# Optimization experiments

Hardware: AMD Instinct MI355X
Metric: run time of the kernel (lower is better)

The kernel has to match this reference:

```python
import jax, jax.numpy as jnp
import numpy as np
from itertools import permutations

SIZES = (16, 32, 32, 32)  # token_sizes for layout dims (v, t, h, w)
N = SIZES[0] * SIZES[1] * SIZES[2] * SIZES[3]  # num_tokens = 524288
B = 32
EPS = 1e-3


def setup_inputs() -> dict:
    key = jax.random.key(0)
    ks = jax.random.split(key, 12)
    u = lambda k, shape: jax.random.uniform(k, shape, dtype=jnp.float32)
    alphas = [1.0, 2.0, 4.0]
    comps = np.array(
        [[alphas[v], alphas[t], alphas[hw], alphas[hw]]
         for v, t, hw in permutations(range(3), 3)], dtype=np.float32)  # [6, 4]
    return {
        "components": jnp.asarray(comps),
        "u_rate_src": u(ks[0], (1,)),
        "u_rate_tgt": u(ks[1], (1,)),
        "u0_src": u(ks[2], (B, N)),
        "u0_tgt": u(ks[3], (B, N)),
        "u_v_src": u(ks[4], (B, SIZES[0])),
        "u_t_src": u(ks[5], (B, SIZES[1])),
        "u_h_src": u(ks[6], (B, SIZES[2])),
        "u_w_src": u(ks[7], (B, SIZES[3])),
        "u_v_tgt": u(ks[8], (B, SIZES[0])),
        "u_t_tgt": u(ks[9], (B, SIZES[1])),
        "u_h_tgt": u(ks[10], (B, SIZES[2])),
        "u_w_tgt": u(ks[11], (B, SIZES[3])),
        "idx": 2,
    }


def _clamp(x):
    return jnp.clip(x, EPS, 1.0 - EPS)


def _binary_mask(u_rate, u0, u_dims, alphas):
    # event_prior: log-prob per token = log U0 + sum_dim log(U_dim)/alpha_dim (broadcast over pattern)
    P = jnp.log(_clamp(u0))  # [B, N]
    for i, ud in enumerate(u_dims):
        shape = [B, 1, 1, 1, 1]
        shape[1 + i] = SIZES[i]
        rep = jnp.broadcast_to(
            (jnp.log(_clamp(ud)) / alphas[i]).reshape(shape),
            (B,) + SIZES).reshape(B, N)
        P = P + rep
    # rate_prior: one shared uniform, K = floor(U * N), expanded over batch
    K = (_clamp(u_rate) * N).astype(jnp.int32)  # [1]
    K = jnp.broadcast_to(K, (B,))[:, None]  # [B, 1]
    # binary_topk_: rank via double argsort (0 = largest), mask = K > rank
    rank = jnp.argsort(jnp.argsort(-P, axis=-1), axis=-1)
    return K > rank


def reference(components, u_rate_src, u_rate_tgt, u0_src, u0_tgt,
              u_v_src, u_t_src, u_h_src, u_w_src,
              u_v_tgt, u_t_tgt, u_h_tgt, u_w_tgt, idx):
    alphas = components[idx]  # [4], one alpha per layout dim, shared by src/tgt
    src = _binary_mask(u_rate_src, u0_src,
                       (u_v_src, u_t_src, u_h_src, u_w_src), alphas)
    tgt = _binary_mask(u_rate_tgt, u0_tgt,
                       (u_v_tgt, u_t_tgt, u_h_tgt, u_w_tgt), alphas)
    return src, tgt
```

## Files before the change

kernel.cpp:

```cpp
#include <hip/hip_runtime.h>
#include <stdint.h>

#define NTOK 524288
#define ROWS 64
#define CHUNKS 64
#define CHUNKS_H 32
#define NTHR 256
#define F4_PER_ROW (NTOK / 4)
#define F4_PER_CHUNK (F4_PER_ROW / CHUNKS)
#define F4_PER_THR (F4_PER_CHUNK / NTHR)
#define F4_PER_CHUNK_H (F4_PER_ROW / CHUNKS_H)
#define F4_PER_THR_H (F4_PER_CHUNK_H / NTHR)
#define NB1 2048
#define B1BASE 30720
#define BCAP 65536
#define GCAP 8192
#define STAGECAP 512

#define OFF_H16  0u
#define OFF_B1   (OFF_H16 + ROWS * NB1 * 4u)
#define OFF_CG   (OFF_B1 + 256u)
#define OFF_BCNT (OFF_CG + 256u)
#define OFF_IT   (OFF_BCNT + 256u)
#define OFF_T    (OFF_IT + 256u)
#define OFF_ZERO_END (OFF_T + 512u)
#define OFF_TAB  OFF_ZERO_END
#define OFF_BK   (OFF_TAB + ROWS * 112u * 8u)
#define OFF_BI   (OFF_BK + (size_t)ROWS * BCAP * 8u)

__device__ __forceinline__ double clamp64(double x) {
  return fmin(fmax(x, 1.0e-3), 1.0 - 1.0e-3);
}

__device__ __forceinline__ unsigned compute_K(float ur) {
  float urf = fminf(fmaxf(ur, 1.0e-3f), 1.0f - 1.0e-3f);
  return (unsigned)(int)(urf * (float)NTOK);
}

__device__ __forceinline__ int bucket16(unsigned long long kb) {
  int b = (int)(unsigned)(kb >> 47) - B1BASE;
  return b < 0 ? 0 : (b > NB1 - 1 ? NB1 - 1 : b);
}

__global__ void k_tables(const float* __restrict__ comps, const int* __restrict__ idxp,
                         const float* __restrict__ uvs, const float* __restrict__ uts,
                         const float* __restrict__ uhs, const float* __restrict__ uws,
                         const float* __restrict__ uvt, const float* __restrict__ utt,
                         const float* __restrict__ uht, const float* __restrict__ uwt,
                         double* __restrict__ tabs) {
  int idx = idxp[0];
  double alpha[4];
  for (int d = 0; d < 4; ++d) alpha[d] = (double)comps[idx * 4 + d];
  for (int i = threadIdx.x; i < ROWS * 112; i += blockDim.x) {
    int row = i / 112, j = i % 112;
    int m = row >> 5, b = row & 31;
    int d, jj, dsz;
    if (j < 16)      { d = 0; jj = j;      dsz = 16; }
    else if (j < 48) { d = 1; jj = j - 16; dsz = 32; }
    else if (j < 80) { d = 2; jj = j - 48; dsz = 32; }
    else             { d = 3; jj = j - 80; dsz = 32; }
    const float* u;
    if (m == 0) u = (d == 0) ? uvs : (d == 1) ? uts : (d == 2) ? uhs : uws;
    else        u = (d == 0) ? uvt : (d == 1) ? utt : (d == 2) ? uht : uwt;
    double x = clamp64((double)u[b * dsz + jj]);
    double a = alpha[d];
    double f;
    if (a == 1.0)      f = x;
    else if (a == 2.0) f = sqrt(x);
    else if (a == 4.0) f = sqrt(sqrt(x));
    else               f = pow(x, 1.0 / a);
    tabs[row * 112 + j] = f;
  }
}

__global__ void k_hist16(const float* __restrict__ u0s, const float* __restrict__ u0t,
                         const double* __restrict__ tabs, unsigned int* __restrict__ h16) {
  __shared__ double tb[112];
  __shared__ unsigned int h[NB1];
  int row = blockIdx.x / CHUNKS_H, chunk = blockIdx.x % CHUNKS_H;
  for (int i = threadIdx.x; i < 112; i += blockDim.x) tb[i] = tabs[row * 112 + i];
  for (int i = threadIdx.x; i < NB1; i += blockDim.x) h[i] = 0;
  __syncthreads();
  int m = row >> 5, b = row & 31;
  const float4* u0 = reinterpret_cast<const float4*>((m ? u0t : u0s) + (size_t)b * NTOK);
  int base = chunk * F4_PER_CHUNK_H;
  for (int it = 0; it < F4_PER_THR_H; ++it) {
    int f4 = base + it * NTHR + threadIdx.x;
    float4 x = u0[f4];
    int n0 = f4 * 4;
    int w0 = n0 & 31, hh = (n0 >> 5) & 31, tt = (n0 >> 10) & 31, vv = n0 >> 15;
    double g = tb[vv] * tb[16 + tt] * tb[48 + hh];
    double k0 = clamp64((double)x.x) * (g * tb[80 + w0 + 0]);
    double k1 = clamp64((double)x.y) * (g * tb[80 + w0 + 1]);
    double k2 = clamp64((double)x.z) * (g * tb[80 + w0 + 2]);
    double k3 = clamp64((double)x.w) * (g * tb[80 + w0 + 3]);
    atomicAdd(&h[bucket16((unsigned long long)__double_as_longlong(k0))], 1u);
    atomicAdd(&h[bucket16((unsigned long long)__double_as_longlong(k1))], 1u);
    atomicAdd(&h[bucket16((unsigned long long)__double_as_longlong(k2))], 1u);
    atomicAdd(&h[bucket16((unsigned long long)__double_as_longlong(k3))], 1u);
  }
  __syncthreads();
  for (int i = threadIdx.x; i < NB1; i += blockDim.x) {
    unsigned c = h[i];
    if (c) atomicAdd(&h16[row * NB1 + i], c);
  }
}

__global__ __launch_bounds__(256) void k_scan16(const unsigned int* __restrict__ h16,
                                                const float* __restrict__ urs,
                                                const float* __restrict__ urt,
                                                int* __restrict__ sB1, int* __restrict__ sCG) {
  __shared__ unsigned suf[256];
  __shared__ int best;
  int row = blockIdx.x;
  int t = threadIdx.x;
  const unsigned* h = h16 + row * NB1;
  unsigned loc[8]; unsigned own = 0;
#pragma unroll
  for (int i = 0; i < 8; ++i) { loc[i] = h[t * 8 + i]; own += loc[i]; }
  suf[t] = own;
  if (t == 0) best = -1;
  __syncthreads();
  for (int off = 1; off < 256; off <<= 1) {
    unsigned add = (t + off < 256) ? suf[t + off] : 0u;
    __syncthreads();
    suf[t] += add;
    __syncthreads();
  }
  int m = row >> 5;
  unsigned K = compute_K(m ? urt[0] : urs[0]);
  unsigned above = suf[t] - own;
  int cand = -1;
  unsigned cum = above;
  for (int i = 7; i >= 0; --i) {
    if (cum + loc[i] >= K) { cand = t * 8 + i; break; }
    cum += loc[i];
  }
  if (cand >= 0) atomicMax(&best, cand);
  __syncthreads();
  int bb = best;
  if (bb >= 0 && (bb >> 3) == t) {
    unsigned cg = above;
    for (int i = 7; i > (bb & 7); --i) cg += loc[i];
    sB1[row] = bb;
    sCG[row] = (int)cg;
  }
}

__global__ void k_gatherw(const float* __restrict__ u0s, const float* __restrict__ u0t,
                          const double* __restrict__ tabs, const int* __restrict__ sB1,
                          unsigned int* __restrict__ bcnt,
                          unsigned long long* __restrict__ bk, unsigned int* __restrict__ bi,
                          int* __restrict__ out) {
  __shared__ double tb[112];
  __shared__ unsigned long long sk[STAGECAP];
  __shared__ unsigned int si[STAGECAP];
  __shared__ unsigned int scnt, sbase;
  int row = blockIdx.x / CHUNKS, chunk = blockIdx.x % CHUNKS;
  for (int i = threadIdx.x; i < 112; i += blockDim.x) tb[i] = tabs[row * 112 + i];
  if (threadIdx.x == 0) scnt = 0;
  __syncthreads();
  int b1 = sB1[row];
  int m = row >> 5, b = row & 31;
  const float4* u0 = reinterpret_cast<const float4*>((m ? u0t : u0s) + (size_t)b * NTOK);
  int4* o = reinterpret_cast<int4*>(out + (size_t)row * NTOK);
  int base = chunk * F4_PER_CHUNK;
  for (int it = 0; it < F4_PER_THR; ++it) {
    int f4 = base + it * NTHR + threadIdx.x;
    float4 x = u0[f4];
    int n0 = f4 * 4;
    int w0 = n0 & 31, hh = (n0 >> 5) & 31, tt = (n0 >> 10) & 31, vv = n0 >> 15;
    double g = tb[vv] * tb[16 + tt] * tb[48 + hh];
    double ks[4];
    ks[0] = clamp64((double)x.x) * (g * tb[80 + w0 + 0]);
    ks[1] = clamp64((double)x.y) * (g * tb[80 + w0 + 1]);
    ks[2] = clamp64((double)x.z) * (g * tb[80 + w0 + 2]);
    ks[3] = clamp64((double)x.w) * (g * tb[80 + w0 + 3]);
    int r[4];
#pragma unroll
    for (int c = 0; c < 4; ++c) {
      unsigned long long kb = (unsigned long long)__double_as_longlong(ks[c]);
      int bkt = bucket16(kb);
      r[c] = (bkt > b1) ? 1 : 0;
      if (bkt == b1) {
        unsigned p = atomicAdd(&scnt, 1u);
        if (p < STAGECAP) { sk[p] = kb; si[p] = (unsigned)(n0 + c); }
        else {
          unsigned gp = atomicAdd(&bcnt[row], 1u);
          if (gp < BCAP) {
            bk[(size_t)row * BCAP + gp] = kb;
            bi[(size_t)row * BCAP + gp] = (unsigned)(n0 + c);
          }
        }
      }
    }
    int4 rv; rv.x = r[0]; rv.y = r[1]; rv.z = r[2]; rv.w = r[3];
    o[f4] = rv;
  }
  __syncthreads();
  unsigned nst = scnt; if (nst > STAGECAP) nst = STAGECAP;
  if (threadIdx.x == 0) sbase = atomicAdd(&bcnt[row], nst);
  __syncthreads();
  unsigned bs = sbase;
  for (unsigned i = threadIdx.x; i < nst; i += blockDim.x) {
    unsigned gp = bs + i;
    if (gp < BCAP) {
      bk[(size_t)row * BCAP + gp] = sk[i];
      bi[(size_t)row * BCAP + gp] = si[i];
    }
  }
}

__global__ __launch_bounds__(256) void k_pick(const unsigned long long* __restrict__ bk,
                                              const unsigned int* __restrict__ bi,
                                              const unsigned int* __restrict__ bcnt,
                                              const float* __restrict__ urs,
                                              const float* __restrict__ urt,
                                              const int* __restrict__ sCG,
                                              unsigned long long* __restrict__ sT,
                                              int* __restrict__ sIT) {
  __shared__ unsigned int h[4096];
  __shared__ unsigned suf[256];
  __shared__ int best;
  __shared__ unsigned long long kk[GCAP];
  __shared__ unsigned int ixx[GCAP];
  __shared__ unsigned int lcnt;
  __shared__ unsigned sharedRem;
  int row = blockIdx.x;
  int t = threadIdx.x;
  unsigned cnt = bcnt[row]; if (cnt > BCAP) cnt = BCAP;
  const unsigned long long* rbk = bk + (size_t)row * BCAP;
  const unsigned int* rbi = bi + (size_t)row * BCAP;
  for (int i = t; i < 4096; i += 256) h[i] = 0;
  if (t == 0) { best = -1; lcnt = 0; }
  __syncthreads();
  for (unsigned i = t; i < cnt; i += 256)
    atomicAdd(&h[(unsigned)(rbk[i] >> 39) & 0xFFFu], 1u);
  __syncthreads();
  unsigned loc[16]; unsigned own = 0;
#pragma unroll
  for (int i = 0; i < 16; ++i) { loc[i] = h[t * 16 + i]; own += loc[i]; }
  suf[t] = own;
  __syncthreads();
  for (int off = 1; off < 256; off <<= 1) {
    unsigned add = (t + off < 256) ? suf[t + off] : 0u;
    __syncthreads();
    suf[t] += add;
    __syncthreads();
  }
  int m = row >> 5;
  unsigned K = compute_K(m ? urt[0] : urs[0]);
  unsigned K2 = K - (unsigned)sCG[row];
  unsigned above = suf[t] - own;
  int cand = -1;
  unsigned cum = above;
  for (int i = 15; i >= 0; --i) {
    if (cum + loc[i] >= K2) { cand = t * 16 + i; break; }
    cum += loc[i];
  }
  if (cand >= 0) atomicMax(&best, cand);
  __syncthreads();
  int b2 = best;
  if (b2 >= 0 && (b2 >> 4) == t) {
    unsigned a2 = above;
    for (int i = 15; i > (b2 & 15); --i) a2 += loc[i];
    sharedRem = K2 - a2;
  }
  __syncthreads();
  unsigned rem = sharedRem;
  for (unsigned i = t; i < cnt; i += 256) {
    unsigned long long kb = rbk[i];
    if (((unsigned)(kb >> 39) & 0xFFFu) == (unsigned)b2) {
      unsigned p = atomicAdd(&lcnt, 1u);
      if (p < GCAP) { kk[p] = kb; ixx[p] = rbi[i]; }
    }
  }
  __syncthreads();
  unsigned n_r = lcnt; if (n_r > GCAP) n_r = GCAP;
  unsigned n2 = 2;
  while (n2 < n_r) n2 <<= 1;
  for (unsigned i = t; i < n2; i += 256)
    if (i >= n_r) { kk[i] = 0ULL; ixx[i] = 0xFFFFFFFFu; }
  __syncthreads();
  for (unsigned kstep = 2; kstep <= n2; kstep <<= 1) {
    for (unsigned j = kstep >> 1; j > 0; j >>= 1) {
      for (int i = t; i < (int)n2; i += 256) {
        int pj = i ^ (int)j;
        if (pj > i) {
          unsigned long long k1 = kk[i], k2v = kk[pj];
          unsigned i1 = ixx[i], i2 = ixx[pj];
          bool bef = (k1 > k2v) || (k1 == k2v && i1 < i2);
          bool dirAsc = ((i & (int)kstep) == 0);
          if (bef != dirAsc) { kk[i] = k2v; kk[pj] = k1; ixx[i] = i2; ixx[pj] = i1; }
        }
      }
      __syncthreads();
    }
  }
  if (t == 0) {
    int r = (int)rem;
    if (r < 1) r = 1;
    if ((unsigned)r > n_r) r = (int)n_r;
    sT[row] = kk[r - 1];
    sIT[row] = (int)ixx[r - 1];
  }
}

__global__ __launch_bounds__(256) void k_fixup(const unsigned long long* __restrict__ bk,
                                               const unsigned int* __restrict__ bi,
                                               const unsigned int* __restrict__ bcnt,
                                               const unsigned long long* __restrict__ sT,
                                               const int* __restrict__ sIT,
                                               int* __restrict__ out) {
  int row = blockIdx.x;
  unsigned cnt = bcnt[row]; if (cnt > BCAP) cnt = BCAP;
  unsigned long long T = sT[row];
  int IT = sIT[row];
  const unsigned long long* rbk = bk + (size_t)row * BCAP;
  const unsigned int* rbi = bi + (size_t)row * BCAP;
  int* o = out + (size_t)row * NTOK;
  for (unsigned i = threadIdx.x; i < cnt; i += blockDim.x) {
    unsigned long long kb = rbk[i];
    unsigned idx = rbi[i];
    o[idx] = (kb > T || (kb == T && (int)idx <= IT)) ? 1 : 0;
  }
}

extern "C" void kernel_launch(void* const* d_in, const int* in_sizes, int n_in,
                              void* d_out, int out_size, void* d_ws, size_t ws_size,
                              hipStream_t stream) {
  const float* comps = (const float*)d_in[0];
  const float* urs   = (const float*)d_in[1];
  const float* urt   = (const float*)d_in[2];
  const float* u0s   = (const float*)d_in[3];
  const float* u0t   = (const float*)d_in[4];
  const float* uvs   = (const float*)d_in[5];
  const float* uts   = (const float*)d_in[6];
  const float* uhs   = (const float*)d_in[7];
  const float* uws   = (const float*)d_in[8];
  const float* uvt   = (const float*)d_in[9];
  const float* utt   = (const float*)d_in[10];
  const float* uht   = (const float*)d_in[11];
  const float* uwt   = (const float*)d_in[12];
  const int*   idxp  = (const int*)d_in[13];
  int* out = (int*)d_out;

  char* ws = (char*)d_ws;
  unsigned int*       h16  = (unsigned int*)(ws + OFF_H16);
  int*                sB1  = (int*)(ws + OFF_B1);
  int*                sCG  = (int*)(ws + OFF_CG);
  unsigned int*       bcnt = (unsigned int*)(ws + OFF_BCNT);
  int*                sIT  = (int*)(ws + OFF_IT);
  unsigned long long* sT   = (unsigned long long*)(ws + OFF_T);
  double*             tabs = (double*)(ws + OFF_TAB);
  unsigned long long* bk   = (unsigned long long*)(ws + OFF_BK);
  unsigned int*       bi   = (unsigned int*)(ws + OFF_BI);

  hipMemsetAsync(d_ws, 0, OFF_ZERO_END, stream);

  k_tables<<<1, 256, 0, stream>>>(comps, idxp, uvs, uts, uhs, uws, uvt, utt, uht, uwt, tabs);
  k_hist16<<<ROWS * CHUNKS_H, NTHR, 0, stream>>>(u0s, u0t, tabs, h16);
  k_scan16<<<ROWS, 256, 0, stream>>>(h16, urs, urt, sB1, sCG);
  k_gatherw<<<ROWS * CHUNKS, NTHR, 0, stream>>>(u0s, u0t, tabs, sB1, bcnt, bk, bi, out);
  k_pick<<<ROWS, 256, 0, stream>>>(bk, bi, bcnt, urs, urt, sCG, sT, sIT);
  k_fixup<<<ROWS, 256, 0, stream>>>(bk, bi, bcnt, sT, sIT, out);
}
```

Baseline: 342.2 us.

## Fuse table build into consumers, merge fixup into pick, replicate histograms

After: 322.3 us. 1.06x faster.

```diff
diff --git a/kernel.cpp b/kernel.cpp
--- a/kernel.cpp
+++ b/kernel.cpp
@@ -12,6 +12,7 @@
 #define F4_PER_CHUNK_H (F4_PER_ROW / CHUNKS_H)
 #define F4_PER_THR_H (F4_PER_CHUNK_H / NTHR)
 #define NB1 2048
+#define NB1R 2052
 #define B1BASE 30720
 #define BCAP 65536
 #define GCAP 8192
@@ -21,11 +22,8 @@
 #define OFF_B1   (OFF_H16 + ROWS * NB1 * 4u)
 #define OFF_CG   (OFF_B1 + 256u)
 #define OFF_BCNT (OFF_CG + 256u)
-#define OFF_IT   (OFF_BCNT + 256u)
-#define OFF_T    (OFF_IT + 256u)
-#define OFF_ZERO_END (OFF_T + 512u)
-#define OFF_TAB  OFF_ZERO_END
-#define OFF_BK   (OFF_TAB + ROWS * 112u * 8u)
+#define OFF_ZERO_END (OFF_BCNT + 256u)
+#define OFF_BK   ((OFF_ZERO_END + 7u) & ~7u)
 #define OFF_BI   (OFF_BK + (size_t)ROWS * BCAP * 8u)
 
 __device__ __forceinline__ double clamp64(double x) {
@@ -42,18 +40,15 @@
   return b < 0 ? 0 : (b > NB1 - 1 ? NB1 - 1 : b);
 }
 
-__global__ void k_tables(const float* __restrict__ comps, const int* __restrict__ idxp,
-                         const float* __restrict__ uvs, const float* __restrict__ uts,
-                         const float* __restrict__ uhs, const float* __restrict__ uws,
-                         const float* __restrict__ uvt, const float* __restrict__ utt,
-                         const float* __restrict__ uht, const float* __restrict__ uwt,
-                         double* __restrict__ tabs) {
+__device__ __forceinline__ void build_tb(double* tb, int row,
+                                         const float* comps, const int* idxp,
+                                         const float* uvs, const float* uts,
+                                         const float* uhs, const float* uws,
+                                         const float* uvt, const float* utt,
+                                         const float* uht, const float* uwt) {
+  int m = row >> 5, b = row & 31;
   int idx = idxp[0];
-  double alpha[4];
-  for (int d = 0; d < 4; ++d) alpha[d] = (double)comps[idx * 4 + d];
-  for (int i = threadIdx.x; i < ROWS * 112; i += blockDim.x) {
-    int row = i / 112, j = i % 112;
-    int m = row >> 5, b = row & 31;
+  for (int j = threadIdx.x; j < 112; j += blockDim.x) {
     int d, jj, dsz;
     if (j < 16)      { d = 0; jj = j;      dsz = 16; }
     else if (j < 48) { d = 1; jj = j - 16; dsz = 32; }
@@ -63,24 +58,30 @@
     if (m == 0) u = (d == 0) ? uvs : (d == 1) ? uts : (d == 2) ? uhs : uws;
     else        u = (d == 0) ? uvt : (d == 1) ? utt : (d == 2) ? uht : uwt;
     double x = clamp64((double)u[b * dsz + jj]);
-    double a = alpha[d];
+    double a = (double)comps[idx * 4 + d];
     double f;
     if (a == 1.0)      f = x;
     else if (a == 2.0) f = sqrt(x);
     else if (a == 4.0) f = sqrt(sqrt(x));
     else               f = pow(x, 1.0 / a);
-    tabs[row * 112 + j] = f;
+    tb[j] = f;
   }
 }
 
 __global__ void k_hist16(const float* __restrict__ u0s, const float* __restrict__ u0t,
-                         const double* __restrict__ tabs, unsigned int* __restrict__ h16) {
+                         const float* __restrict__ comps, const int* __restrict__ idxp,
+                         const float* __restrict__ uvs, const float* __restrict__ uts,
+                         const float* __restrict__ uhs, const float* __restrict__ uws,
+                         const float* __restrict__ uvt, const float* __restrict__ utt,
+                         const float* __restrict__ uht, const float* __restrict__ uwt,
+                         unsigned int* __restrict__ h16) {
   __shared__ double tb[112];
-  __shared__ unsigned int h[NB1];
+  __shared__ unsigned int h[2 * NB1R];
   int row = blockIdx.x / CHUNKS_H, chunk = blockIdx.x % CHUNKS_H;
-  for (int i = threadIdx.x; i < 112; i += blockDim.x) tb[i] = tabs[row * 112 + i];
-  for (int i = threadIdx.x; i < NB1; i += blockDim.x) h[i] = 0;
-  __syncthreads();
+  build_tb(tb, row, comps, idxp, uvs, uts, uhs, uws, uvt, utt, uht, uwt);
+  for (int i = threadIdx.x; i < 2 * NB1R; i += blockDim.x) h[i] = 0;
+  __syncthreads();
+  unsigned rep = (threadIdx.x & 1) * NB1R;
   int m = row >> 5, b = row & 31;
   const float4* u0 = reinterpret_cast<const float4*>((m ? u0t : u0s) + (size_t)b * NTOK);
   int base = chunk * F4_PER_CHUNK_H;
@@ -94,14 +95,14 @@
     double k1 = clamp64((double)x.y) * (g * tb[80 + w0 + 1]);
     double k2 = clamp64((double)x.z) * (g * tb[80 + w0 + 2]);
     double k3 = clamp64((double)x.w) * (g * tb[80 + w0 + 3]);
-    atomicAdd(&h[bucket16((unsigned long long)__double_as_longlong(k0))], 1u);
-    atomicAdd(&h[bucket16((unsigned long long)__double_as_longlong(k1))], 1u);
-    atomicAdd(&h[bucket16((unsigned long long)__double_as_longlong(k2))], 1u);
-    atomicAdd(&h[bucket16((unsigned long long)__double_as_longlong(k3))], 1u);
+    atomicAdd(&h[rep + bucket16((unsigned long long)__double_as_longlong(k0))], 1u);
+    atomicAdd(&h[rep + bucket16((unsigned long long)__double_as_longlong(k1))], 1u);
+    atomicAdd(&h[rep + bucket16((unsigned long long)__double_as_longlong(k2))], 1u);
+    atomicAdd(&h[rep + bucket16((unsigned long long)__double_as_longlong(k3))], 1u);
   }
   __syncthreads();
   for (int i = threadIdx.x; i < NB1; i += blockDim.x) {
-    unsigned c = h[i];
+    unsigned c = h[i] + h[NB1R + i];
     if (c) atomicAdd(&h16[row * NB1 + i], c);
   }
 }
@@ -148,7 +149,12 @@
 }
 
 __global__ void k_gatherw(const float* __restrict__ u0s, const float* __restrict__ u0t,
-                          const double* __restrict__ tabs, const int* __restrict__ sB1,
+                          const float* __restrict__ comps, const int* __restrict__ idxp,
+                          const float* __restrict__ uvs, const float* __restrict__ uts,
+                          const float* __restrict__ uhs, const float* __restrict__ uws,
+                          const float* __restrict__ uvt, const float* __restrict__ utt,
+                          const float* __restrict__ uht, const float* __restrict__ uwt,
+                          const int* __restrict__ sB1,
                           unsigned int* __restrict__ bcnt,
                           unsigned long long* __restrict__ bk, unsigned int* __restrict__ bi,
                           int* __restrict__ out) {
@@ -157,7 +163,7 @@
   __shared__ unsigned int si[STAGECAP];
   __shared__ unsigned int scnt, sbase;
   int row = blockIdx.x / CHUNKS, chunk = blockIdx.x % CHUNKS;
-  for (int i = threadIdx.x; i < 112; i += blockDim.x) tb[i] = tabs[row * 112 + i];
+  build_tb(tb, row, comps, idxp, uvs, uts, uhs, uws, uvt, utt, uht, uwt);
   if (threadIdx.x == 0) scnt = 0;
   __syncthreads();
   int b1 = sB1[row];
@@ -217,8 +223,7 @@
                                               const float* __restrict__ urs,
                                               const float* __restrict__ urt,
                                               const int* __restrict__ sCG,
-                                              unsigned long long* __restrict__ sT,
-                                              int* __restrict__ sIT) {
+                                              int* __restrict__ out) {
   __shared__ unsigned int h[4096];
   __shared__ unsigned suf[256];
   __shared__ int best;
@@ -226,6 +231,8 @@
   __shared__ unsigned int ixx[GCAP];
   __shared__ unsigned int lcnt;
   __shared__ unsigned sharedRem;
+  __shared__ unsigned long long shT;
+  __shared__ int shIT;
   int row = blockIdx.x;
   int t = threadIdx.x;
   unsigned cnt = bcnt[row]; if (cnt > BCAP) cnt = BCAP;
@@ -301,25 +308,14 @@
     int r = (int)rem;
     if (r < 1) r = 1;
     if ((unsigned)r > n_r) r = (int)n_r;
-    sT[row] = kk[r - 1];
-    sIT[row] = (int)ixx[r - 1];
-  }
-}
-
-__global__ __launch_bounds__(256) void k_fixup(const unsigned long long* __restrict__ bk,
-                                               const unsigned int* __restrict__ bi,
-                                               const unsigned int* __restrict__ bcnt,
-                                               const unsigned long long* __restrict__ sT,
-                                               const int* __restrict__ sIT,
-                                               int* __restrict__ out) {
-  int row = blockIdx.x;
-  unsigned cnt = bcnt[row]; if (cnt > BCAP) cnt = BCAP;
-  unsigned long long T = sT[row];
-  int IT = sIT[row];
-  const unsigned long long* rbk = bk + (size_t)row * BCAP;
-  const unsigned int* rbi = bi + (size_t)row * BCAP;
+    shT = kk[r - 1];
+    shIT = (int)ixx[r - 1];
+  }
+  __syncthreads();
+  unsigned long long T = shT;
+  int IT = shIT;
   int* o = out + (size_t)row * NTOK;
-  for (unsigned i = threadIdx.x; i < cnt; i += blockDim.x) {
+  for (unsigned i = t; i < cnt; i += 256) {
     unsigned long long kb = rbk[i];
     unsigned idx = rbi[i];
     o[idx] = (kb > T || (kb == T && (int)idx <= IT)) ? 1 : 0;
@@ -350,18 +346,16 @@
   int*                sB1  = (int*)(ws + OFF_B1);
   int*                sCG  = (int*)(ws + OFF_CG);
   unsigned int*       bcnt = (unsigned int*)(ws + OFF_BCNT);
-  int*                sIT  = (int*)(ws + OFF_IT);
-  unsigned long long* sT   = (unsigned long long*)(ws + OFF_T);
-  double*             tabs = (double*)(ws + OFF_TAB);
   unsigned long long* bk   = (unsigned long long*)(ws + OFF_BK);
   unsigned int*       bi   = (unsigned int*)(ws + OFF_BI);
 
   hipMemsetAsync(d_ws, 0, OFF_ZERO_END, stream);
 
-  k_tables<<<1, 256, 0, stream>>>(comps, idxp, uvs, uts, uhs, uws, uvt, utt, uht, uwt, tabs);
-  k_hist16<<<ROWS * CHUNKS_H, NTHR, 0, stream>>>(u0s, u0t, tabs, h16);
+  k_hist16<<<ROWS * CHUNKS_H, NTHR, 0, stream>>>(u0s, u0t, comps, idxp,
+                                                 uvs, uts, uhs, uws, uvt, utt, uht, uwt, h16);
   k_scan16<<<ROWS, 256, 0, stream>>>(h16, urs, urt, sB1, sCG);
-  k_gatherw<<<ROWS * CHUNKS, NTHR, 0, stream>>>(u0s, u0t, tabs, sB1, bcnt, bk, bi, out);
-  k_pick<<<ROWS, 256, 0, stream>>>(bk, bi, bcnt, urs, urt, sCG, sT, sIT);
-  k_fixup<<<ROWS, 256, 0, stream>>>(bk, bi, bcnt, sT, sIT, out);
-}
+  k_gatherw<<<ROWS * CHUNKS, NTHR, 0, stream>>>(u0s, u0t, comps, idxp,
+                                                uvs, uts, uhs, uws, uvt, utt, uht, uwt,
+                                                sB1, bcnt, bk, bi, out);
+  k_pick<<<ROWS, 256, 0, stream>>>(bk, bi, bcnt, urs, urt, sCG, out);
+}
```
